# Kernel optimization log

Measured on AMD Instinct MI355X. Metric: run time of the kernel, lower is better.

## Reference

```python
import jax, jax.numpy as jnp
import numpy as np

B, L, D = 64, 4096, 256

def setup_inputs() -> dict:
    key = jax.random.key(0)
    k1, k2 = jax.random.split(key)
    inp = jax.random.normal(k1, (B, L, D), dtype=jnp.float32)
    # lengths in [1, L] so no empty-sequence mean (matches original assumption)
    length = jax.random.randint(k2, (B,), 1, L + 1, dtype=jnp.int64)
    return {"input": inp, "length": length}

def reference(input, length):
    # One fused masked mean over the ragged sequence dim.
    # mask: [B, L] True for valid positions
    mask = (jnp.arange(input.shape[1])[None, :] < length[:, None])
    m = mask.astype(input.dtype)[:, :, None]            # [B, L, 1]
    summed = jnp.sum(input * m, axis=1)                  # [B, D]
    return summed / length.astype(input.dtype)[:, None] # [B, D]
```

## Files before the change

kernel.cpp:

```cpp
#include <hip/hip_runtime.h>

#define BB 64
#define LL 4096
#define DD 256
#define PP 64
#define ROWS_PER_CHUNK (LL / PP)
#define D4 (DD / 4)

__global__ __launch_bounds__(64) void avg_partial_kernel(
    const float* __restrict__ in,
    const int* __restrict__ len,
    float* __restrict__ ws)
{
    const int b    = blockIdx.x / PP;
    const int p    = blockIdx.x % PP;
    const int lane = threadIdx.x;

    const int lb   = len[b];
    const int row0 = p * ROWS_PER_CHUNK;
    int rend = row0 + ROWS_PER_CHUNK;
    if (rend > lb) rend = (lb > row0) ? lb : row0;

    float4 acc = make_float4(0.f, 0.f, 0.f, 0.f);
    const float4* __restrict__ base =
        (const float4*)(in + (size_t)b * LL * DD);

    for (int r = row0; r < rend; ++r) {
        float4 v = base[(size_t)r * D4 + lane];
        acc.x += v.x; acc.y += v.y; acc.z += v.z; acc.w += v.w;
    }

    float4* __restrict__ wsb = (float4*)ws + ((size_t)b * PP + p) * D4;
    wsb[lane] = acc;
}

__global__ __launch_bounds__(64) void avg_reduce_kernel(
    const float* __restrict__ ws,
    const int* __restrict__ len,
    float* __restrict__ out)
{
    const int b    = blockIdx.x;
    const int lane = threadIdx.x;

    float4 acc = make_float4(0.f, 0.f, 0.f, 0.f);
    const float4* __restrict__ wsb = (const float4*)ws + (size_t)b * PP * D4;

    #pragma unroll 4
    for (int p = 0; p < PP; ++p) {
        float4 v = wsb[(size_t)p * D4 + lane];
        acc.x += v.x; acc.y += v.y; acc.z += v.z; acc.w += v.w;
    }

    int lb = len[b];
    if (lb < 1) lb = 1;
    const float inv = 1.0f / (float)lb;
    float4 o = make_float4(acc.x * inv, acc.y * inv, acc.z * inv, acc.w * inv);
    ((float4*)out)[(size_t)b * D4 + lane] = o;
}

__global__ void avg_zero_out_kernel(float* __restrict__ out) {
    int i = blockIdx.x * blockDim.x + threadIdx.x;
    if (i < BB * DD) out[i] = 0.f;
}

__global__ __launch_bounds__(64) void avg_atomic_kernel(
    const float* __restrict__ in,
    const int* __restrict__ len,
    float* __restrict__ out)
{
    const int b    = blockIdx.x / PP;
    const int p    = blockIdx.x % PP;
    const int lane = threadIdx.x;

    int lb = len[b];
    if (lb < 1) lb = 1;
    const int row0 = p * ROWS_PER_CHUNK;
    int rend = row0 + ROWS_PER_CHUNK;
    if (rend > lb) rend = (lb > row0) ? lb : row0;
    if (rend <= row0) return;

    float4 acc = make_float4(0.f, 0.f, 0.f, 0.f);
    const float4* __restrict__ base = (const float4*)(in + (size_t)b * LL * DD);
    for (int r = row0; r < rend; ++r) {
        float4 v = base[(size_t)r * D4 + lane];
        acc.x += v.x; acc.y += v.y; acc.z += v.z; acc.w += v.w;
    }
    const float inv = 1.0f / (float)lb;
    float* o = out + (size_t)b * DD + lane * 4;
    atomicAdd(o + 0, acc.x * inv);
    atomicAdd(o + 1, acc.y * inv);
    atomicAdd(o + 2, acc.z * inv);
    atomicAdd(o + 3, acc.w * inv);
}

extern "C" void kernel_launch(void* const* d_in, const int* in_sizes, int n_in,
                              void* d_out, int out_size, void* d_ws, size_t ws_size,
                              hipStream_t stream) {
    const float* in  = (const float*)d_in[0];
    const int*   len = (const int*)d_in[1];
    float*       out = (float*)d_out;

    const size_t ws_needed = (size_t)BB * PP * DD * sizeof(float);

    if (ws_size >= ws_needed && d_ws != nullptr) {
        float* ws = (float*)d_ws;
        avg_partial_kernel<<<BB * PP, 64, 0, stream>>>(in, len, ws);
        avg_reduce_kernel<<<BB, 64, 0, stream>>>(ws, len, out);
    } else {
        avg_zero_out_kernel<<<(BB * DD + 255) / 256, 256, 0, stream>>>(out);
        avg_atomic_kernel<<<BB * PP, 64, 0, stream>>>(in, len, out);
    }
}
```

Measured before the change: 35.77 us.

## Pack four waves per block, skip empty chunks, parallelize reduce across waves

The partial kernel now runs four 64-lane waves per 256-thread block, and waves whose chunk lies beyond the sequence length exit without writing. The reduce kernel reads only the chunks that are valid, splits them across four waves and combines the four partial sums through shared memory. The row loop is unrolled by eight to keep more loads in flight. The aim is to cut block-launch overhead, skip workspace writes and reads for empty chunks, and speed up the serial reduction, at the cost of a shared-memory sync and possible tail imbalance inside blocks.

After: 33.79 us. 5.5% less time.

```diff
diff --git a/kernel.cpp b/kernel.cpp
--- a/kernel.cpp
+++ b/kernel.cpp
@@ -6,25 +6,31 @@
 #define PP 64
 #define ROWS_PER_CHUNK (LL / PP)
 #define D4 (DD / 4)
+#define WAVES 4
 
-__global__ __launch_bounds__(64) void avg_partial_kernel(
+__global__ __launch_bounds__(256) void avg_partial_kernel(
     const float* __restrict__ in,
     const int* __restrict__ len,
     float* __restrict__ ws)
 {
-    const int b    = blockIdx.x / PP;
-    const int p    = blockIdx.x % PP;
-    const int lane = threadIdx.x;
+    const int w    = threadIdx.x >> 6;
+    const int lane = threadIdx.x & 63;
+    const int c    = blockIdx.x * WAVES + w;
+    const int b    = c >> 6;
+    const int p    = c & 63;
 
-    const int lb   = len[b];
+    const int lb      = len[b];
+    const int nchunks = (lb + ROWS_PER_CHUNK - 1) >> 6;
+    if (p >= nchunks) return;
+
     const int row0 = p * ROWS_PER_CHUNK;
     int rend = row0 + ROWS_PER_CHUNK;
-    if (rend > lb) rend = (lb > row0) ? lb : row0;
+    if (rend > lb) rend = lb;
 
     float4 acc = make_float4(0.f, 0.f, 0.f, 0.f);
-    const float4* __restrict__ base =
-        (const float4*)(in + (size_t)b * LL * DD);
+    const float4* __restrict__ base = (const float4*)(in + (size_t)b * LL * DD);
 
+    #pragma unroll 8
     for (int r = row0; r < rend; ++r) {
         float4 v = base[(size_t)r * D4 + lane];
         acc.x += v.x; acc.y += v.y; acc.z += v.z; acc.w += v.w;
@@ -34,28 +40,41 @@
     wsb[lane] = acc;
 }
 
-__global__ __launch_bounds__(64) void avg_reduce_kernel(
+__global__ __launch_bounds__(256) void avg_reduce_kernel(
     const float* __restrict__ ws,
     const int* __restrict__ len,
     float* __restrict__ out)
 {
     const int b    = blockIdx.x;
-    const int lane = threadIdx.x;
+    const int w    = threadIdx.x >> 6;
+    const int lane = threadIdx.x & 63;
+
+    int lb = len[b];
+    if (lb < 1) lb = 1;
+    const int nchunks = (lb + ROWS_PER_CHUNK - 1) >> 6;
 
     float4 acc = make_float4(0.f, 0.f, 0.f, 0.f);
     const float4* __restrict__ wsb = (const float4*)ws + (size_t)b * PP * D4;
 
-    #pragma unroll 4
-    for (int p = 0; p < PP; ++p) {
+    for (int p = w; p < nchunks; p += WAVES) {
         float4 v = wsb[(size_t)p * D4 + lane];
         acc.x += v.x; acc.y += v.y; acc.z += v.z; acc.w += v.w;
     }
 
-    int lb = len[b];
-    if (lb < 1) lb = 1;
-    const float inv = 1.0f / (float)lb;
-    float4 o = make_float4(acc.x * inv, acc.y * inv, acc.z * inv, acc.w * inv);
-    ((float4*)out)[(size_t)b * D4 + lane] = o;
+    __shared__ float4 sh[WAVES - 1][64];
+    if (w > 0) sh[w - 1][lane] = acc;
+    __syncthreads();
+
+    if (w == 0) {
+        #pragma unroll
+        for (int i = 0; i < WAVES - 1; ++i) {
+            float4 v = sh[i][lane];
+            acc.x += v.x; acc.y += v.y; acc.z += v.z; acc.w += v.w;
+        }
+        const float inv = 1.0f / (float)lb;
+        float4 o = make_float4(acc.x * inv, acc.y * inv, acc.z * inv, acc.w * inv);
+        ((float4*)out)[(size_t)b * D4 + lane] = o;
+    }
 }
 
 __global__ void avg_zero_out_kernel(float* __restrict__ out) {
@@ -104,8 +123,8 @@
 
     if (ws_size >= ws_needed && d_ws != nullptr) {
         float* ws = (float*)d_ws;
-        avg_partial_kernel<<<BB * PP, 64, 0, stream>>>(in, len, ws);
-        avg_reduce_kernel<<<BB, 64, 0, stream>>>(ws, len, out);
+        avg_partial_kernel<<<(BB * PP) / WAVES, 256, 0, stream>>>(in, len, ws);
+        avg_reduce_kernel<<<BB, 256, 0, stream>>>(ws, len, out);
     } else {
         avg_zero_out_kernel<<<(BB * DD + 255) / 256, 256, 0, stream>>>(out);
         avg_atomic_kernel<<<BB * PP, 64, 0, stream>>>(in, len, out);
```

## Fuse partial and final reduction into one atomic kernel with block-level LDS combine

Applied to the files above, without the earlier changes.

Replaces the two-kernel workspace reduction with a single kernel. Each 256-thread block runs four wavefronts over 32-row chunks, combines their results through shared memory, and issues float atomics into an output that a memset clears first. Blocks whose rows lie past the sequence length exit early, and the row loop is unrolled by 8. This removes the workspace write and read-back and the second kernel launch, at the cost of atomic contention, a memset, and a summation order that is no longer deterministic.

Result: faster. 31.84 us (-11.0%).

```diff
diff --git a/kernel.cpp b/kernel.cpp
--- a/kernel.cpp
+++ b/kernel.cpp
@@ -3,94 +3,60 @@
 #define BB 64
 #define LL 4096
 #define DD 256
-#define PP 64
-#define ROWS_PER_CHUNK (LL / PP)
 #define D4 (DD / 4)
+#define PP 128
+#define RPC (LL / PP)
+#define CPB 4
+#define BPB (PP / CPB)
 
-__global__ __launch_bounds__(64) void avg_partial_kernel(
-    const float* __restrict__ in,
-    const int* __restrict__ len,
-    float* __restrict__ ws)
-{
-    const int b    = blockIdx.x / PP;
-    const int p    = blockIdx.x % PP;
-    const int lane = threadIdx.x;
-
-    const int lb   = len[b];
-    const int row0 = p * ROWS_PER_CHUNK;
-    int rend = row0 + ROWS_PER_CHUNK;
-    if (rend > lb) rend = (lb > row0) ? lb : row0;
-
-    float4 acc = make_float4(0.f, 0.f, 0.f, 0.f);
-    const float4* __restrict__ base =
-        (const float4*)(in + (size_t)b * LL * DD);
-
-    for (int r = row0; r < rend; ++r) {
-        float4 v = base[(size_t)r * D4 + lane];
-        acc.x += v.x; acc.y += v.y; acc.z += v.z; acc.w += v.w;
-    }
-
-    float4* __restrict__ wsb = (float4*)ws + ((size_t)b * PP + p) * D4;
-    wsb[lane] = acc;
-}
-
-__global__ __launch_bounds__(64) void avg_reduce_kernel(
-    const float* __restrict__ ws,
-    const int* __restrict__ len,
-    float* __restrict__ out)
-{
-    const int b    = blockIdx.x;
-    const int lane = threadIdx.x;
-
-    float4 acc = make_float4(0.f, 0.f, 0.f, 0.f);
-    const float4* __restrict__ wsb = (const float4*)ws + (size_t)b * PP * D4;
-
-    #pragma unroll 4
-    for (int p = 0; p < PP; ++p) {
-        float4 v = wsb[(size_t)p * D4 + lane];
-        acc.x += v.x; acc.y += v.y; acc.z += v.z; acc.w += v.w;
-    }
-
-    int lb = len[b];
-    if (lb < 1) lb = 1;
-    const float inv = 1.0f / (float)lb;
-    float4 o = make_float4(acc.x * inv, acc.y * inv, acc.z * inv, acc.w * inv);
-    ((float4*)out)[(size_t)b * D4 + lane] = o;
-}
-
-__global__ void avg_zero_out_kernel(float* __restrict__ out) {
-    int i = blockIdx.x * blockDim.x + threadIdx.x;
-    if (i < BB * DD) out[i] = 0.f;
-}
-
-__global__ __launch_bounds__(64) void avg_atomic_kernel(
+__global__ __launch_bounds__(256) void avg_fused_kernel(
     const float* __restrict__ in,
     const int* __restrict__ len,
     float* __restrict__ out)
 {
-    const int b    = blockIdx.x / PP;
-    const int p    = blockIdx.x % PP;
-    const int lane = threadIdx.x;
+    const int w      = threadIdx.x >> 6;
+    const int lane   = threadIdx.x & 63;
+    const int b      = blockIdx.x / BPB;
+    const int blockp = blockIdx.x % BPB;
 
     int lb = len[b];
     if (lb < 1) lb = 1;
-    const int row0 = p * ROWS_PER_CHUNK;
-    int rend = row0 + ROWS_PER_CHUNK;
-    if (rend > lb) rend = (lb > row0) ? lb : row0;
-    if (rend <= row0) return;
+
+    if (blockp * (CPB * RPC) >= lb) return;
+
+    const int p    = blockp * CPB + w;
+    const int row0 = p * RPC;
 
     float4 acc = make_float4(0.f, 0.f, 0.f, 0.f);
-    const float4* __restrict__ base = (const float4*)(in + (size_t)b * LL * DD);
-    for (int r = row0; r < rend; ++r) {
-        float4 v = base[(size_t)r * D4 + lane];
-        acc.x += v.x; acc.y += v.y; acc.z += v.z; acc.w += v.w;
+    if (row0 < lb) {
+        int n = lb - row0;
+        if (n > RPC) n = RPC;
+        const float4* __restrict__ base =
+            (const float4*)(in + (size_t)b * LL * DD) + (size_t)row0 * D4 + lane;
+        #pragma unroll 8
+        for (int r = 0; r < n; ++r) {
+            float4 v = base[(size_t)r * D4];
+            acc.x += v.x; acc.y += v.y; acc.z += v.z; acc.w += v.w;
+        }
     }
-    const float inv = 1.0f / (float)lb;
-    float* o = out + (size_t)b * DD + lane * 4;
-    atomicAdd(o + 0, acc.x * inv);
-    atomicAdd(o + 1, acc.y * inv);
-    atomicAdd(o + 2, acc.z * inv);
-    atomicAdd(o + 3, acc.w * inv);
+
+    __shared__ float4 sh[CPB - 1][64];
+    if (w > 0) sh[w - 1][lane] = acc;
+    __syncthreads();
+
+    if (w == 0) {
+        #pragma unroll
+        for (int i = 0; i < CPB - 1; ++i) {
+            float4 v = sh[i][lane];
+            acc.x += v.x; acc.y += v.y; acc.z += v.z; acc.w += v.w;
+        }
+        const float inv = 1.0f / (float)lb;
+        float* __restrict__ o = out + (size_t)b * DD + lane * 4;
+        atomicAdd(o + 0, acc.x * inv);
+        atomicAdd(o + 1, acc.y * inv);
+        atomicAdd(o + 2, acc.z * inv);
+        atomicAdd(o + 3, acc.w * inv);
+    }
 }
 
 extern "C" void kernel_launch(void* const* d_in, const int* in_sizes, int n_in,
@@ -100,14 +66,7 @@
     const int*   len = (const int*)d_in[1];
     float*       out = (float*)d_out;
 
-    const size_t ws_needed = (size_t)BB * PP * DD * sizeof(float);
+    hipMemsetAsync(out, 0, (size_t)out_size * sizeof(float), stream);
 
-    if (ws_size >= ws_needed && d_ws != nullptr) {
-        float* ws = (float*)d_ws;
-        avg_partial_kernel<<<BB * PP, 64, 0, stream>>>(in, len, ws);
-        avg_reduce_kernel<<<BB, 64, 0, stream>>>(ws, len, out);
-    } else {
-        avg_zero_out_kernel<<<(BB * DD + 255) / 256, 256, 0, stream>>>(out);
-        avg_atomic_kernel<<<BB * PP, 64, 0, stream>>>(in, len, out);
-    }
+    avg_fused_kernel<<<BB * BPB, 256, 0, stream>>>(in, len, out);
 }
```
